# Kernel tuning notes

Hardware: AMD Instinct MI355X
Metric: run time of the kernel (lower is better)

The kernel has to match this reference:

```python
import jax, jax.numpy as jnp
import numpy as np

B = 8388608  # batch rows
IN, OUT = 3, 3

def setup_inputs() -> dict:
    key = jax.random.key(0)
    k1, k2, k3 = jax.random.split(key, 3)
    x = jax.random.normal(k1, (B, IN), dtype=jnp.float32) * 5.0  # spread so clamping triggers
    bound = 1.0 / np.sqrt(IN)
    W = jax.random.uniform(k2, (OUT, IN), dtype=jnp.float32, minval=-bound, maxval=bound)
    b = jax.random.uniform(k3, (OUT,), dtype=jnp.float32, minval=-bound, maxval=bound)
    return {"x": x, "W": W, "b": b}

def reference(x, W, b):
    # vectorized physics sim: pos, vel, action = x[:,0], x[:,1], x[:,2]
    vel = x[:, 1] + x[:, 2]
    pos = x[:, 0] + vel
    hit_wall = (pos > 10.0) | (pos < -10.0)
    vel = jnp.where(hit_wall, -vel, vel)
    pos = jnp.clip(pos, -10.0, 10.0)
    reward = -pos * pos
    prediction = jnp.stack([pos, vel, reward], axis=-1)  # [B, 3]
    y = x @ W.T + b  # tiny Linear, [B, 3]
    return prediction + 1e-10 * y
```

## Files before the change

kernel.cpp:

```cpp
#include <hip/hip_runtime.h>


__device__ __forceinline__ void sim_row(float x0, float x1, float x2,
                                        const float* Wv, const float* bv,
                                        float& pos_o, float& vel_o, float& rew_o) {
    float vel = x1 + x2;
    float pos = x0 + vel;
    bool hit = (pos > 10.0f) || (pos < -10.0f);
    vel = hit ? -vel : vel;
    pos = fminf(10.0f, fmaxf(-10.0f, pos));
    float reward = -pos * pos;
    float y0 = fmaf(x0, Wv[0], fmaf(x1, Wv[1], fmaf(x2, Wv[2], bv[0])));
    float y1 = fmaf(x0, Wv[3], fmaf(x1, Wv[4], fmaf(x2, Wv[5], bv[1])));
    float y2 = fmaf(x0, Wv[6], fmaf(x1, Wv[7], fmaf(x2, Wv[8], bv[2])));
    pos_o = fmaf(1e-10f, y0, pos);
    vel_o = fmaf(1e-10f, y1, vel);
    rew_o = fmaf(1e-10f, y2, reward);
}

__global__ __launch_bounds__(256) void HitTheMiddleModel_kernel(
        const float4* __restrict__ X4,
        const float* __restrict__ W,
        const float* __restrict__ B,
        float4* __restrict__ O4,
        const float* __restrict__ X,
        float* __restrict__ O,
        int n4, int rem) {
    int q = blockIdx.x * blockDim.x + threadIdx.x;

    float Wv[9];
#pragma unroll
    for (int i = 0; i < 9; ++i) Wv[i] = W[i];
    float bv[3] = {B[0], B[1], B[2]};

    if (q < n4) {
        int iL = (q > 0) ? q - 1 : 0;
        int iR = (q < n4 - 1) ? q + 1 : q;
        float4 Lv = X4[iL];
        float4 Cv = X4[q];
        float4 Rv = X4[iR];
        float w0 = Lv.x, w1 = Lv.y, w2 = Lv.z, w3 = Lv.w;
        float w4 = Cv.x, w5 = Cv.y, w6 = Cv.z, w7 = Cv.w;
        float w8 = Rv.x, w9 = Rv.y;

        int m = q % 3;
        float4 r;
        float pA, vA, rA, pB, vB, rB;
        if (m == 0) {
            sim_row(w4, w5, w6, Wv, bv, pA, vA, rA);
            sim_row(w7, w8, w9, Wv, bv, pB, vB, rB);
            r = make_float4(pA, vA, rA, pB);
        } else if (m == 1) {
            sim_row(w3, w4, w5, Wv, bv, pA, vA, rA);
            sim_row(w6, w7, w8, Wv, bv, pB, vB, rB);
            r = make_float4(vA, rA, pB, vB);
        } else {
            sim_row(w2, w3, w4, Wv, bv, pA, vA, rA);
            sim_row(w5, w6, w7, Wv, bv, pB, vB, rB);
            r = make_float4(rA, pB, vB, rB);
        }
        O4[q] = r;
    } else if (q < n4 + rem) {
        long long g = 4LL * n4 + (q - n4);
        long long row = g / 3;
        int c = (int)(g % 3);
        float x0 = X[3 * row], x1 = X[3 * row + 1], x2 = X[3 * row + 2];
        float p, v, rw;
        sim_row(x0, x1, x2, Wv, bv, p, v, rw);
        O[g] = (c == 0) ? p : (c == 1) ? v : rw;
    }
}

extern "C" void kernel_launch(void* const* d_in, const int* in_sizes, int n_in,
                              void* d_out, int out_size, void* d_ws, size_t ws_size,
                              hipStream_t stream) {
    const float* x = (const float*)d_in[0];
    const float* W = (const float*)d_in[1];
    const float* b = (const float*)d_in[2];
    float* out = (float*)d_out;

    long long nfloats = (long long)in_sizes[0];
    long long n4 = nfloats / 4;
    int rem = (int)(nfloats - 4 * n4);

    long long nthreads = n4 + rem;
    const int block = 256;
    long long grid = (nthreads + block - 1) / block;

    HitTheMiddleModel_kernel<<<(int)grid, block, 0, stream>>>(
        (const float4*)x, W, b, (float4*)out, x, out, (int)n4, rem);
}
```

Measured before the change: 177.4 us.

## Stage row blocks through LDS to avoid redundant neighbor float4 loads

Replaces the per-thread three-float4 halo loads (left, center, right) with a cooperative coalesced float4 load of a block's 1024 rows into shared memory. Each thread then computes four rows from LDS, writes the results back in place, and the block stores them as coalesced float4s. A separate tail kernel handles leftover floats. This cuts redundant global reads, which were tripled (though mostly cache hits), at the cost of LDS traffic, two barriers and stride-3 LDS accesses that may cause bank conflicts.

```diff
diff --git a/kernel.cpp b/kernel.cpp
--- a/kernel.cpp
+++ b/kernel.cpp
@@ -1,5 +1,10 @@
 #include <hip/hip_runtime.h>
 
+
+#define BLOCK 256
+#define R_PER_T 4
+#define ROWS_PER_BLOCK (BLOCK * R_PER_T)
+#define F4_PER_BLOCK (ROWS_PER_BLOCK * 3 / 4)
 
 __device__ __forceinline__ void sim_row(float x0, float x1, float x2,
                                         const float* Wv, const float* bv,
@@ -18,57 +23,70 @@
     rew_o = fmaf(1e-10f, y2, reward);
 }
 
-__global__ __launch_bounds__(256) void HitTheMiddleModel_kernel(
+__global__ __launch_bounds__(BLOCK) void HitTheMiddleModel_kernel(
         const float4* __restrict__ X4,
         const float* __restrict__ W,
         const float* __restrict__ B,
         float4* __restrict__ O4,
-        const float* __restrict__ X,
-        float* __restrict__ O,
-        int n4, int rem) {
-    int q = blockIdx.x * blockDim.x + threadIdx.x;
+        long long n4, long long safeRows) {
+    __shared__ float4 lds4[F4_PER_BLOCK];
+    float* ldsf = (float*)lds4;
+
+    const int t = threadIdx.x;
+    const long long f4base = (long long)blockIdx.x * F4_PER_BLOCK;
+    const long long rowbase = (long long)blockIdx.x * ROWS_PER_BLOCK;
 
     float Wv[9];
 #pragma unroll
     for (int i = 0; i < 9; ++i) Wv[i] = W[i];
     float bv[3] = {B[0], B[1], B[2]};
 
-    if (q < n4) {
-        int iL = (q > 0) ? q - 1 : 0;
-        int iR = (q < n4 - 1) ? q + 1 : q;
-        float4 Lv = X4[iL];
-        float4 Cv = X4[q];
-        float4 Rv = X4[iR];
-        float w0 = Lv.x, w1 = Lv.y, w2 = Lv.z, w3 = Lv.w;
-        float w4 = Cv.x, w5 = Cv.y, w6 = Cv.z, w7 = Cv.w;
-        float w8 = Rv.x, w9 = Rv.y;
+#pragma unroll
+    for (int k = 0; k < 3; ++k) {
+        long long g = f4base + t + k * BLOCK;
+        if (g < n4) lds4[t + k * BLOCK] = X4[g];
+    }
+    __syncthreads();
 
-        int m = q % 3;
-        float4 r;
-        float pA, vA, rA, pB, vB, rB;
-        if (m == 0) {
-            sim_row(w4, w5, w6, Wv, bv, pA, vA, rA);
-            sim_row(w7, w8, w9, Wv, bv, pB, vB, rB);
-            r = make_float4(pA, vA, rA, pB);
-        } else if (m == 1) {
-            sim_row(w3, w4, w5, Wv, bv, pA, vA, rA);
-            sim_row(w6, w7, w8, Wv, bv, pB, vB, rB);
-            r = make_float4(vA, rA, pB, vB);
-        } else {
-            sim_row(w2, w3, w4, Wv, bv, pA, vA, rA);
-            sim_row(w5, w6, w7, Wv, bv, pB, vB, rB);
-            r = make_float4(rA, pB, vB, rB);
+#pragma unroll
+    for (int k = 0; k < R_PER_T; ++k) {
+        int lr = t + k * BLOCK;
+        long long row = rowbase + lr;
+        if (row < safeRows) {
+            float x0 = ldsf[3 * lr + 0];
+            float x1 = ldsf[3 * lr + 1];
+            float x2 = ldsf[3 * lr + 2];
+            float p, v, rw;
+            sim_row(x0, x1, x2, Wv, bv, p, v, rw);
+            ldsf[3 * lr + 0] = p;
+            ldsf[3 * lr + 1] = v;
+            ldsf[3 * lr + 2] = rw;
         }
-        O4[q] = r;
-    } else if (q < n4 + rem) {
-        long long g = 4LL * n4 + (q - n4);
-        long long row = g / 3;
-        int c = (int)(g % 3);
-        float x0 = X[3 * row], x1 = X[3 * row + 1], x2 = X[3 * row + 2];
-        float p, v, rw;
-        sim_row(x0, x1, x2, Wv, bv, p, v, rw);
-        O[g] = (c == 0) ? p : (c == 1) ? v : rw;
     }
+    __syncthreads();
+
+#pragma unroll
+    for (int k = 0; k < 3; ++k) {
+        long long g = f4base + t + k * BLOCK;
+        if (g < n4) O4[g] = lds4[t + k * BLOCK];
+    }
+}
+
+__global__ void HitTheMiddleModel_tail(
+        const float* __restrict__ X, const float* __restrict__ W,
+        const float* __restrict__ B, float* __restrict__ O,
+        long long startFloat, long long nfloats) {
+    long long g = startFloat + blockIdx.x * blockDim.x + threadIdx.x;
+    if (g >= nfloats) return;
+    float Wv[9];
+    for (int i = 0; i < 9; ++i) Wv[i] = W[i];
+    float bv[3] = {B[0], B[1], B[2]};
+    long long row = g / 3;
+    int c = (int)(g % 3);
+    float x0 = X[3 * row], x1 = X[3 * row + 1], x2 = X[3 * row + 2];
+    float p, v, rw;
+    sim_row(x0, x1, x2, Wv, bv, p, v, rw);
+    O[g] = (c == 0) ? p : (c == 1) ? v : rw;
 }
 
 extern "C" void kernel_launch(void* const* d_in, const int* in_sizes, int n_in,
@@ -80,13 +98,20 @@
     float* out = (float*)d_out;
 
     long long nfloats = (long long)in_sizes[0];
+    long long rows = nfloats / 3;
     long long n4 = nfloats / 4;
-    int rem = (int)(nfloats - 4 * n4);
+    long long safeRows = (4 * n4) / 3;
+    if (safeRows > rows) safeRows = rows;
 
-    long long nthreads = n4 + rem;
-    const int block = 256;
-    long long grid = (nthreads + block - 1) / block;
+    long long grid = (rows + ROWS_PER_BLOCK - 1) / ROWS_PER_BLOCK;
+    HitTheMiddleModel_kernel<<<(int)grid, BLOCK, 0, stream>>>(
+        (const float4*)x, W, b, (float4*)out, n4, safeRows);
 
-    HitTheMiddleModel_kernel<<<(int)grid, block, 0, stream>>>(
-        (const float4*)x, W, b, (float4*)out, x, out, (int)n4, rem);
+    long long startFloat = 3 * safeRows;
+    if (startFloat < nfloats) {
+        long long tailN = nfloats - startFloat;
+        int tgrid = (int)((tailN + 255) / 256);
+        HitTheMiddleModel_tail<<<tgrid, 256, 0, stream>>>(
+            x, W, b, out, startFloat, nfloats);
+    }
 }
```

Measured after the change: 179.7 us. Within noise of the previous version (+1.3%).
